# Performance work log

Measured on AMD Instinct MI355X. Metric: run time of the kernel, lower is better.

Reference implementation:

```python
import jax, jax.numpy as jnp
import numpy as np

NQ, NP, E, D, H = 100000, 200000, 500000, 128, 128


def setup_inputs() -> dict:
    key = jax.random.key(0)
    ks = jax.random.split(key, 13)
    ri = lambda k, n: jax.random.randint(k, (E,), 0, n, dtype=jnp.int32)
    return {
        "x_query": jax.random.normal(ks[0], (NQ, D), jnp.float32),
        "x_product": jax.random.normal(ks[1], (NP, D), jnp.float32),
        # [layer, relation, in, out]; relations ordered as ALL_TYPES:
        # 0=Click(Q->P), 1=reverse_Click(P->Q), 2=reverse_QueryResult(P->Q), 3=QueryResult(Q->P)
        "W_self": jax.random.normal(ks[2], (2, 4, D, H), jnp.float32) / np.sqrt(D).astype(np.float32),
        "W_neigh": jax.random.normal(ks[3], (2, 4, D, H), jnp.float32) / np.sqrt(D).astype(np.float32),
        "bias": jax.random.normal(ks[4], (2, 4, H), jnp.float32) * 0.01,
        "click_src": ri(ks[5], NQ), "click_dst": ri(ks[6], NP),
        "qres_src": ri(ks[7], NQ), "qres_dst": ri(ks[8], NP),
        "rclick_src": ri(ks[9], NP), "rclick_dst": ri(ks[10], NQ),
        "rqres_src": ri(ks[11], NP), "rqres_dst": ri(ks[12], NQ),
    }


def _sage(h_src, h_dst, src, dst, n_dst, Ws, Wn, b):
    # DGL SAGEConv 'mean': fc_self(h_dst) + fc_neigh(mean over in-neighbors) + bias
    msum = jax.ops.segment_sum(h_src[src], dst, num_segments=n_dst)  # [n_dst, D]
    deg = jax.ops.segment_sum(jnp.ones(src.shape, h_src.dtype), dst, num_segments=n_dst)
    mean = msum / jnp.maximum(deg, 1.0)[:, None]  # zero-degree nodes get 0
    return h_dst @ Ws + mean @ Wn + b


def reference(x_query, x_product, W_self, W_neigh, bias,
              click_src, click_dst, qres_src, qres_dst,
              rclick_src, rclick_dst, rqres_src, rqres_dst):
    hQ, hP = x_query, x_product
    for l in range(2):
        # HeteroGraphConv aggregate='sum' over relations sharing a dst type
        newP = (_sage(hQ, hP, click_src, click_dst, NP, W_self[l, 0], W_neigh[l, 0], bias[l, 0])
                + _sage(hQ, hP, qres_src, qres_dst, NP, W_self[l, 3], W_neigh[l, 3], bias[l, 3]))
        newQ = (_sage(hP, hQ, rclick_src, rclick_dst, NQ, W_self[l, 1], W_neigh[l, 1], bias[l, 1])
                + _sage(hP, hQ, rqres_src, rqres_dst, NQ, W_self[l, 2], W_neigh[l, 2], bias[l, 2]))
        if l == 0:  # ReLU on all ntypes except after last layer
            newQ, newP = jax.nn.relu(newQ), jax.nn.relu(newP)
        hQ, hP = newQ, newP
    return hQ, hP
```

## Files before the change

kernel.cpp:

```cpp
#include <hip/hip_runtime.h>
#include <hip/hip_bf16.h>

typedef __hip_bfloat16 bf16;
typedef __attribute__((ext_vector_type(8))) short bfrag8;
typedef __attribute__((ext_vector_type(4))) float facc4;

#define NQ_ 100000
#define NP_ 200000
#define NE_ 500000

static __device__ __forceinline__ short f2bf_bits(float f) {
    bf16 h = __float2bfloat16(f);
    short r;
    __builtin_memcpy(&r, &h, 2);
    return r;
}

static __device__ __forceinline__ float bfbits2f(unsigned u) {
    return __builtin_bit_cast(float, u);
}

static __device__ __forceinline__ void store_val(bf16* p, float v) { *p = __float2bfloat16(v); }
static __device__ __forceinline__ void store_val(float* p, float v) { *p = v; }

__global__ void cast_all(const float* __restrict__ xq, const float* __restrict__ xp,
                         bf16* __restrict__ xqb, bf16* __restrict__ xpb) {
    int i = blockIdx.x * blockDim.x + threadIdx.x;
    const int nq4 = NQ_ * 32;
    float4 v;
    short4 o;
    if (i < nq4) {
        v = reinterpret_cast<const float4*>(xq)[i];
        o.x = f2bf_bits(v.x); o.y = f2bf_bits(v.y); o.z = f2bf_bits(v.z); o.w = f2bf_bits(v.w);
        reinterpret_cast<short4*>(xqb)[i] = o;
    } else {
        int j = i - nq4;
        if (j >= NP_ * 32) return;
        v = reinterpret_cast<const float4*>(xp)[j];
        o.x = f2bf_bits(v.x); o.y = f2bf_bits(v.y); o.z = f2bf_bits(v.z); o.w = f2bf_bits(v.w);
        reinterpret_cast<short4*>(xpb)[j] = o;
    }
}

__global__ void prep_weights(const float* __restrict__ Wself, const float* __restrict__ Wneigh,
                             bf16* __restrict__ Wt) {
    int g = blockIdx.x * blockDim.x + threadIdx.x;
    if (g >= 12 * 16384) return;
    int m = g >> 14;
    int rem = g & 16383;
    int n = rem >> 7, k = rem & 127;
    int l = m / 6, t = (m / 3) % 2, s = m % 3;
    int rA = (t == 0) ? 0 : 1;
    int rB = (t == 0) ? 3 : 2;
    float v;
    if (s == 0) {
        v = Wself[((size_t)(l * 4 + rA) * 128 + k) * 128 + n]
          + Wself[((size_t)(l * 4 + rB) * 128 + k) * 128 + n];
    } else {
        int r = (s == 1) ? rA : rB;
        v = Wneigh[((size_t)(l * 4 + r) * 128 + k) * 128 + n];
    }
    Wt[(size_t)m * 16384 + n * 128 + k] = __float2bfloat16(v);
}

__global__ void prep_bias(const float* __restrict__ bias, float* __restrict__ bsum) {
    int g = blockIdx.x * blockDim.x + threadIdx.x;
    if (g >= 512) return;
    int l = g >> 8, t = (g >> 7) & 1, n = g & 127;
    int rA = (t == 0) ? 0 : 1;
    int rB = (t == 0) ? 3 : 2;
    bsum[g] = bias[(l * 4 + rA) * 128 + n] + bias[(l * 4 + rB) * 128 + n];
}


#define NE4_ (NE_ / 4)

__global__ void deg_count_all(const int* __restrict__ cdst, const int* __restrict__ qdst,
                              const int* __restrict__ rcdst, const int* __restrict__ rqdst,
                              int* __restrict__ degAll) {
    int t = blockIdx.x * blockDim.x + threadIdx.x;
    if (t >= 4 * NE4_) return;
    int rel = t / NE4_;
    int er = (t - rel * NE4_) * 4;
    const int* dsts; int base;
    if (rel == 0)      { dsts = cdst;  base = 0; }
    else if (rel == 1) { dsts = qdst;  base = NP_; }
    else if (rel == 2) { dsts = rcdst; base = 2 * NP_; }
    else               { dsts = rqdst; base = 2 * NP_ + NQ_; }
    int4 d4 = *reinterpret_cast<const int4*>(dsts + er);
    atomicAdd(degAll + base + d4.x, 1);
    atomicAdd(degAll + base + d4.y, 1);
    atomicAdd(degAll + base + d4.z, 1);
    atomicAdd(degAll + base + d4.w, 1);
}

__global__ void scan1(const int* __restrict__ deg, int* __restrict__ offs,
                      int* __restrict__ partials, int n) {
    __shared__ int sdata[256];
    int base = blockIdx.x * 1024;
    int t = threadIdx.x;
    int v[4]; int s = 0;
    for (int j = 0; j < 4; ++j) {
        int i = base + t * 4 + j;
        v[j] = (i < n) ? deg[i] : 0;
        s += v[j];
    }
    sdata[t] = s;
    __syncthreads();
    for (int d2 = 1; d2 < 256; d2 <<= 1) {
        int x = (t >= d2) ? sdata[t - d2] : 0;
        __syncthreads();
        sdata[t] += x;
        __syncthreads();
    }
    int excl = sdata[t] - s;
    if (t == 255) partials[blockIdx.x] = sdata[255];
    int run = excl;
    for (int j = 0; j < 4; ++j) {
        int i = base + t * 4 + j;
        if (i < n) offs[i] = run;
        run += v[j];
    }
}

__global__ void scan2(int* __restrict__ partials, int nparts) {
    __shared__ int sdata[256];
    int t = threadIdx.x;
    int v[4]; int s = 0;
    for (int j = 0; j < 4; ++j) {
        int i = t * 4 + j;
        v[j] = (i < nparts) ? partials[i] : 0;
        s += v[j];
    }
    sdata[t] = s;
    __syncthreads();
    for (int d2 = 1; d2 < 256; d2 <<= 1) {
        int x = (t >= d2) ? sdata[t - d2] : 0;
        __syncthreads();
        sdata[t] += x;
        __syncthreads();
    }
    int excl = sdata[t] - s;
    int run = excl;
    for (int j = 0; j < 4; ++j) {
        int i = t * 4 + j;
        if (i < nparts) partials[i] = run;
        run += v[j];
    }
}

__global__ void scan3(int* __restrict__ offs, int* __restrict__ cur,
                      const int* __restrict__ partials, int n) {
    int i = blockIdx.x * blockDim.x + threadIdx.x;
    if (i < n) {
        int v = offs[i] + partials[i >> 10];
        offs[i] = v;
        cur[i] = v;
    }
}

__global__ void csr_fill_all(const int* __restrict__ csrc, const int* __restrict__ cdst,
                             const int* __restrict__ qsrc, const int* __restrict__ qdst,
                             const int* __restrict__ rcsrc, const int* __restrict__ rcdst,
                             const int* __restrict__ rqsrc, const int* __restrict__ rqdst,
                             int* __restrict__ curAll, int* __restrict__ bukAll) {
    int t = blockIdx.x * blockDim.x + threadIdx.x;
    if (t >= 4 * NE4_) return;
    int rel = t / NE4_;
    int er = (t - rel * NE4_) * 4;
    const int* srcs; const int* dsts; int base;
    if (rel == 0)      { srcs = csrc;  dsts = cdst;  base = 0; }
    else if (rel == 1) { srcs = qsrc;  dsts = qdst;  base = NP_; }
    else if (rel == 2) { srcs = rcsrc; dsts = rcdst; base = 2 * NP_; }
    else               { srcs = rqsrc; dsts = rqdst; base = 2 * NP_ + NQ_; }
    int4 d4 = *reinterpret_cast<const int4*>(dsts + er);
    int4 s4 = *reinterpret_cast<const int4*>(srcs + er);
    int p0 = atomicAdd(curAll + base + d4.x, 1);
    int p1 = atomicAdd(curAll + base + d4.y, 1);
    int p2 = atomicAdd(curAll + base + d4.z, 1);
    int p3 = atomicAdd(curAll + base + d4.w, 1);
    bukAll[p0] = s4.x;
    bukAll[p1] = s4.y;
    bukAll[p2] = s4.z;
    bukAll[p3] = s4.w;
}

__global__ __launch_bounds__(256, 8)
void gather_all(const bf16* __restrict__ hQ, const bf16* __restrict__ hP,
                const int* __restrict__ bukAll, const int* __restrict__ offAll,
                const int* __restrict__ degAll, bf16* __restrict__ meanAll) {
    const int tid = threadIdx.x;
    const int lane = tid & 63;
    const int g = lane >> 4;
    const int li = lane & 15;
    const int w = blockIdx.x * 16 + (tid >> 6) * 4 + g;
    const bf16* h = (w < 2 * NP_) ? hQ : hP;
    const int beg = offAll[w];
    const int cnt = degAll[w];

    float a0 = 0.f, a1 = 0.f, a2 = 0.f, a3 = 0.f, a4 = 0.f, a5 = 0.f, a6 = 0.f, a7 = 0.f;

    int myidx = (li < cnt) ? bukAll[beg + li] : 0;
    const int c16 = (cnt < 16) ? cnt : 16;
    const int last = c16 - 1;
    for (int i = 0; i < c16; i += 4) {
#pragma unroll
        for (int j = 0; j < 4; ++j) {
            int idx = i + j;
            int src_lane = g * 16 + ((idx < c16) ? idx : last);
            float m = (idx < c16) ? 1.0f : 0.0f;
            int s_ = __shfl(myidx, src_lane);
            int4 v = reinterpret_cast<const int4*>(h + (size_t)s_ * 128)[li];
            unsigned u0 = (unsigned)v.x, u1 = (unsigned)v.y, u2 = (unsigned)v.z, u3 = (unsigned)v.w;
            a0 = fmaf(bfbits2f(u0 << 16), m, a0);
            a1 = fmaf(bfbits2f(u0 & 0xffff0000u), m, a1);
            a2 = fmaf(bfbits2f(u1 << 16), m, a2);
            a3 = fmaf(bfbits2f(u1 & 0xffff0000u), m, a3);
            a4 = fmaf(bfbits2f(u2 << 16), m, a4);
            a5 = fmaf(bfbits2f(u2 & 0xffff0000u), m, a5);
            a6 = fmaf(bfbits2f(u3 << 16), m, a6);
            a7 = fmaf(bfbits2f(u3 & 0xffff0000u), m, a7);
        }
    }
    for (int i = 16; i < cnt; ++i) {
        int s_ = bukAll[beg + i];
        int4 v = reinterpret_cast<const int4*>(h + (size_t)s_ * 128)[li];
        unsigned u0 = (unsigned)v.x, u1 = (unsigned)v.y, u2 = (unsigned)v.z, u3 = (unsigned)v.w;
        a0 += bfbits2f(u0 << 16);
        a1 += bfbits2f(u0 & 0xffff0000u);
        a2 += bfbits2f(u1 << 16);
        a3 += bfbits2f(u1 & 0xffff0000u);
        a4 += bfbits2f(u2 << 16);
        a5 += bfbits2f(u2 & 0xffff0000u);
        a6 += bfbits2f(u3 << 16);
        a7 += bfbits2f(u3 & 0xffff0000u);
    }

    float r = (cnt > 0) ? (1.0f / (float)cnt) : 0.0f;
    unsigned o0 = ((unsigned)(unsigned short)f2bf_bits(a1 * r) << 16) | (unsigned short)f2bf_bits(a0 * r);
    unsigned o1 = ((unsigned)(unsigned short)f2bf_bits(a3 * r) << 16) | (unsigned short)f2bf_bits(a2 * r);
    unsigned o2 = ((unsigned)(unsigned short)f2bf_bits(a5 * r) << 16) | (unsigned short)f2bf_bits(a4 * r);
    unsigned o3 = ((unsigned)(unsigned short)f2bf_bits(a7 * r) << 16) | (unsigned short)f2bf_bits(a6 * r);
    int4 ov;
    ov.x = (int)o0; ov.y = (int)o1; ov.z = (int)o2; ov.w = (int)o3;
    reinterpret_cast<int4*>(meanAll + (size_t)w * 128)[li] = ov;
}

template <typename OT>
__global__ __launch_bounds__(256, 3)
void sage_all(const bf16* __restrict__ hQin, const bf16* __restrict__ hPin,
              const bf16* __restrict__ meanAll, const bf16* __restrict__ WtL,
              const float* __restrict__ bsumL,
              OT* __restrict__ outQ, OT* __restrict__ outP,
              int do_relu, int nblkP) {
    __shared__ short lA[64 * 136];
    const int tid = threadIdx.x;
    const int wave = tid >> 6, lane = tid & 63;
    const int i16 = lane & 15, quad = lane >> 4;

    const bool isP = (int)blockIdx.x < nblkP;
    const int blk = isP ? blockIdx.x : blockIdx.x - nblkP;
    const int row0 = blk * 64;
    const int nrows = isP ? NP_ : NQ_;
    const bf16* hdst = isP ? hPin : hQin;
    const bf16* m1 = meanAll + (isP ? (size_t)0 : (size_t)(2 * NP_)) * 128;
    const bf16* m2 = meanAll + (isP ? (size_t)NP_ : (size_t)(2 * NP_ + NQ_)) * 128;
    const bf16* Wt3 = WtL + (size_t)(isP ? 0 : 3) * 16384;
    const float* bs = bsumL + (isP ? 0 : 128);
    OT* out = isP ? outP : outQ;

    facc4 acc[4][2];
    for (int nt = 0; nt < 2; ++nt) {
        float bv = bs[wave * 32 + nt * 16 + i16];
        for (int mt = 0; mt < 4; ++mt) {
            facc4 a = {bv, bv, bv, bv};
            acc[mt][nt] = a;
        }
    }

    const bf16* Asrc[3] = {hdst, m1, m2};
#pragma unroll
    for (int s = 0; s < 3; ++s) {
        __syncthreads();
        {
            const bf16* A = Asrc[s];
            for (int j = 0; j < 4; ++j) {
                int c = j * 256 + tid;
                int r = c >> 4, k = (c & 15) * 8;
                int grow = row0 + r;
                int4 v = {0, 0, 0, 0};
                if (grow < nrows)
                    v = reinterpret_cast<const int4*>(A)[((size_t)grow * 128 + k) >> 3];
                *reinterpret_cast<int4*>(&lA[r * 136 + k]) = v;
            }
        }
        __syncthreads();
        const bf16* Ws = Wt3 + (size_t)s * 16384;
#pragma unroll
        for (int k0 = 0; k0 < 128; k0 += 32) {
            bfrag8 a[4], b[2];
            for (int mt = 0; mt < 4; ++mt)
                a[mt] = *reinterpret_cast<const bfrag8*>(&lA[(mt * 16 + i16) * 136 + k0 + quad * 8]);
            for (int nt = 0; nt < 2; ++nt)
                b[nt] = *reinterpret_cast<const bfrag8*>(
                    Ws + (size_t)(wave * 32 + nt * 16 + i16) * 128 + k0 + quad * 8);
            for (int mt = 0; mt < 4; ++mt)
                for (int nt = 0; nt < 2; ++nt)
                    acc[mt][nt] = __builtin_amdgcn_mfma_f32_16x16x32_bf16(a[mt], b[nt], acc[mt][nt], 0, 0, 0);
        }
    }

    for (int mt = 0; mt < 4; ++mt) {
        for (int nt = 0; nt < 2; ++nt) {
            int n = wave * 32 + nt * 16 + i16;
            for (int r = 0; r < 4; ++r) {
                int m = mt * 16 + quad * 4 + r;
                int grow = row0 + m;
                if (grow < nrows) {
                    float v = acc[mt][nt][r];
                    if (do_relu) v = fmaxf(v, 0.0f);
                    store_val(out + (size_t)grow * 128 + n, v);
                }
            }
        }
    }
}


extern "C" void kernel_launch(void* const* d_in, const int* in_sizes, int n_in,
                              void* d_out, int out_size, void* d_ws, size_t ws_size,
                              hipStream_t stream) {
    const float* xq     = (const float*)d_in[0];
    const float* xp     = (const float*)d_in[1];
    const float* Wself  = (const float*)d_in[2];
    const float* Wneigh = (const float*)d_in[3];
    const float* bias   = (const float*)d_in[4];
    const int* csrc  = (const int*)d_in[5];
    const int* cdst  = (const int*)d_in[6];
    const int* qsrc  = (const int*)d_in[7];
    const int* qdst  = (const int*)d_in[8];
    const int* rcsrc = (const int*)d_in[9];
    const int* rcdst = (const int*)d_in[10];
    const int* rqsrc = (const int*)d_in[11];
    const int* rqdst = (const int*)d_in[12];

    const int NDST = 2 * NP_ + 2 * NQ_;

    char* w = (char*)d_ws;
    bf16* xqb    = (bf16*)w;  w += (size_t)NQ_ * 128 * 2;
    bf16* xpb    = (bf16*)w;  w += (size_t)NP_ * 128 * 2;
    bf16* hQ1    = (bf16*)w;  w += (size_t)NQ_ * 128 * 2;
    bf16* hP1    = (bf16*)w;  w += (size_t)NP_ * 128 * 2;
    bf16* meanAll = (bf16*)w; w += (size_t)NDST * 128 * 2;
    bf16* Wt     = (bf16*)w;  w += (size_t)12 * 16384 * 2;
    float* bsum  = (float*)w; w += 512 * 4;
    int* degAll  = (int*)w;   w += (size_t)NDST * 4;
    int* offAll  = (int*)w;   w += (size_t)NDST * 4;
    int* curAll  = (int*)w;   w += (size_t)NDST * 4;
    int* bukAll  = (int*)w;   w += (size_t)4 * NE_ * 4;
    int* partials = (int*)w;  w += 1024 * 4;

    float* outQ = (float*)d_out;
    float* outP = outQ + (size_t)NQ_ * 128;

    cast_all<<<((NQ_ + NP_) * 32 + 255) / 256, 256, 0, stream>>>(xq, xp, xqb, xpb);
    prep_weights<<<768, 256, 0, stream>>>(Wself, Wneigh, Wt);
    prep_bias<<<2, 256, 0, stream>>>(bias, bsum);

    hipMemsetAsync(degAll, 0, (size_t)NDST * 4, stream);
    deg_count_all<<<(4 * NE4_ + 255) / 256, 256, 0, stream>>>(cdst, qdst, rcdst, rqdst, degAll);
    int nparts = (NDST + 1023) / 1024;
    scan1<<<nparts, 256, 0, stream>>>(degAll, offAll, partials, NDST);
    scan2<<<1, 256, 0, stream>>>(partials, nparts);
    scan3<<<(NDST + 255) / 256, 256, 0, stream>>>(offAll, curAll, partials, NDST);
    csr_fill_all<<<(4 * NE4_ + 255) / 256, 256, 0, stream>>>(csrc, cdst, qsrc, qdst,
                                                             rcsrc, rcdst, rqsrc, rqdst,
                                                             curAll, bukAll);

    const int nblkP = (NP_ + 63) / 64;
    const int nblkQ = (NQ_ + 63) / 64;
    const int gather_blocks = NDST / 16;

    for (int l = 0; l < 2; ++l) {
        const bf16* hQin = l ? hQ1 : xqb;
        const bf16* hPin = l ? hP1 : xpb;
        const bf16* WtL = Wt + (size_t)l * 6 * 16384;
        const float* bL = bsum + l * 256;

        gather_all<<<gather_blocks, 256, 0, stream>>>(hQin, hPin, bukAll, offAll, degAll, meanAll);

        if (l == 0)
            sage_all<bf16><<<nblkP + nblkQ, 256, 0, stream>>>(hQin, hPin, meanAll, WtL, bL,
                                                              hQ1, hP1, 1, nblkP);
        else
            sage_all<float><<<nblkP + nblkQ, 256, 0, stream>>>(hQin, hPin, meanAll, WtL, bL,
                                                               outQ, outP, 0, nblkP);
    }
}
```

Before: 897.6 us.

## Fuse preprocessing launches and record per-edge ranks to drop second atomic pass

Merges the cast and degree-count kernels into one launch, and the CSR fill, weight prep and bias prep into another, cutting the launch count. The degree-count pass now saves each edge's atomic return value as its rank, so the fill pass writes to offset+rank with no second round of atomics and scan3 no longer copies a cursor array. The cost is an extra 8 MB rank buffer that must be written and read back, and edges are now handled one per thread instead of four per thread with int4 loads.

```diff
diff --git a/kernel.cpp b/kernel.cpp
--- a/kernel.cpp
+++ b/kernel.cpp
@@ -8,6 +8,11 @@
 #define NQ_ 100000
 #define NP_ 200000
 #define NE_ 500000
+
+#define CAST_BLOCKS 37500
+#define EDGE_BLOCKS 7813
+#define PREPW_BLOCKS 768
+#define PREPB_BLOCKS 2
 
 static __device__ __forceinline__ short f2bf_bits(float f) {
     bf16 h = __float2bfloat16(f);
@@ -23,76 +28,40 @@
 static __device__ __forceinline__ void store_val(bf16* p, float v) { *p = __float2bfloat16(v); }
 static __device__ __forceinline__ void store_val(float* p, float v) { *p = v; }
 
-__global__ void cast_all(const float* __restrict__ xq, const float* __restrict__ xp,
-                         bf16* __restrict__ xqb, bf16* __restrict__ xpb) {
-    int i = blockIdx.x * blockDim.x + threadIdx.x;
-    const int nq4 = NQ_ * 32;
-    float4 v;
-    short4 o;
-    if (i < nq4) {
-        v = reinterpret_cast<const float4*>(xq)[i];
-        o.x = f2bf_bits(v.x); o.y = f2bf_bits(v.y); o.z = f2bf_bits(v.z); o.w = f2bf_bits(v.w);
-        reinterpret_cast<short4*>(xqb)[i] = o;
-    } else {
-        int j = i - nq4;
-        if (j >= NP_ * 32) return;
-        v = reinterpret_cast<const float4*>(xp)[j];
-        o.x = f2bf_bits(v.x); o.y = f2bf_bits(v.y); o.z = f2bf_bits(v.z); o.w = f2bf_bits(v.w);
-        reinterpret_cast<short4*>(xpb)[j] = o;
-    }
-}
-
-__global__ void prep_weights(const float* __restrict__ Wself, const float* __restrict__ Wneigh,
-                             bf16* __restrict__ Wt) {
-    int g = blockIdx.x * blockDim.x + threadIdx.x;
-    if (g >= 12 * 16384) return;
-    int m = g >> 14;
-    int rem = g & 16383;
-    int n = rem >> 7, k = rem & 127;
-    int l = m / 6, t = (m / 3) % 2, s = m % 3;
-    int rA = (t == 0) ? 0 : 1;
-    int rB = (t == 0) ? 3 : 2;
-    float v;
-    if (s == 0) {
-        v = Wself[((size_t)(l * 4 + rA) * 128 + k) * 128 + n]
-          + Wself[((size_t)(l * 4 + rB) * 128 + k) * 128 + n];
-    } else {
-        int r = (s == 1) ? rA : rB;
-        v = Wneigh[((size_t)(l * 4 + r) * 128 + k) * 128 + n];
-    }
-    Wt[(size_t)m * 16384 + n * 128 + k] = __float2bfloat16(v);
-}
-
-__global__ void prep_bias(const float* __restrict__ bias, float* __restrict__ bsum) {
-    int g = blockIdx.x * blockDim.x + threadIdx.x;
-    if (g >= 512) return;
-    int l = g >> 8, t = (g >> 7) & 1, n = g & 127;
-    int rA = (t == 0) ? 0 : 1;
-    int rB = (t == 0) ? 3 : 2;
-    bsum[g] = bias[(l * 4 + rA) * 128 + n] + bias[(l * 4 + rB) * 128 + n];
-}
-
-
-#define NE4_ (NE_ / 4)
-
-__global__ void deg_count_all(const int* __restrict__ cdst, const int* __restrict__ qdst,
-                              const int* __restrict__ rcdst, const int* __restrict__ rqdst,
-                              int* __restrict__ degAll) {
-    int t = blockIdx.x * blockDim.x + threadIdx.x;
-    if (t >= 4 * NE4_) return;
-    int rel = t / NE4_;
-    int er = (t - rel * NE4_) * 4;
-    const int* dsts; int base;
-    if (rel == 0)      { dsts = cdst;  base = 0; }
-    else if (rel == 1) { dsts = qdst;  base = NP_; }
-    else if (rel == 2) { dsts = rcdst; base = 2 * NP_; }
-    else               { dsts = rqdst; base = 2 * NP_ + NQ_; }
-    int4 d4 = *reinterpret_cast<const int4*>(dsts + er);
-    atomicAdd(degAll + base + d4.x, 1);
-    atomicAdd(degAll + base + d4.y, 1);
-    atomicAdd(degAll + base + d4.z, 1);
-    atomicAdd(degAll + base + d4.w, 1);
-}
+__global__ void fused_cast_deg(const float* __restrict__ xq, const float* __restrict__ xp,
+                               bf16* __restrict__ xqb, bf16* __restrict__ xpb,
+                               const int* __restrict__ cdst, const int* __restrict__ qdst,
+                               const int* __restrict__ rcdst, const int* __restrict__ rqdst,
+                               int* __restrict__ degAll, int* __restrict__ rankAll) {
+    if ((int)blockIdx.x < CAST_BLOCKS) {
+        int i = blockIdx.x * blockDim.x + threadIdx.x;
+        const int nq4 = NQ_ * 32;
+        float4 v;
+        short4 o;
+        if (i < nq4) {
+            v = reinterpret_cast<const float4*>(xq)[i];
+            o.x = f2bf_bits(v.x); o.y = f2bf_bits(v.y); o.z = f2bf_bits(v.z); o.w = f2bf_bits(v.w);
+            reinterpret_cast<short4*>(xqb)[i] = o;
+        } else {
+            int j = i - nq4;
+            v = reinterpret_cast<const float4*>(xp)[j];
+            o.x = f2bf_bits(v.x); o.y = f2bf_bits(v.y); o.z = f2bf_bits(v.z); o.w = f2bf_bits(v.w);
+            reinterpret_cast<short4*>(xpb)[j] = o;
+        }
+        return;
+    }
+    int e = (blockIdx.x - CAST_BLOCKS) * blockDim.x + threadIdx.x;
+    if (e >= 4 * NE_) return;
+    int rel = e / NE_;
+    int er = e - rel * NE_;
+    int d, base;
+    if (rel == 0)      { d = cdst[er];  base = 0; }
+    else if (rel == 1) { d = qdst[er];  base = NP_; }
+    else if (rel == 2) { d = rcdst[er]; base = 2 * NP_; }
+    else               { d = rqdst[er]; base = 2 * NP_ + NQ_; }
+    rankAll[e] = atomicAdd(degAll + base + d, 1);
+}
+
 
 __global__ void scan1(const int* __restrict__ deg, int* __restrict__ offs,
                       int* __restrict__ partials, int n) {
@@ -149,40 +118,60 @@
     }
 }
 
-__global__ void scan3(int* __restrict__ offs, int* __restrict__ cur,
-                      const int* __restrict__ partials, int n) {
+__global__ void scan3(int* __restrict__ offs, const int* __restrict__ partials, int n) {
     int i = blockIdx.x * blockDim.x + threadIdx.x;
-    if (i < n) {
-        int v = offs[i] + partials[i >> 10];
-        offs[i] = v;
-        cur[i] = v;
-    }
-}
-
-__global__ void csr_fill_all(const int* __restrict__ csrc, const int* __restrict__ cdst,
-                             const int* __restrict__ qsrc, const int* __restrict__ qdst,
-                             const int* __restrict__ rcsrc, const int* __restrict__ rcdst,
-                             const int* __restrict__ rqsrc, const int* __restrict__ rqdst,
-                             int* __restrict__ curAll, int* __restrict__ bukAll) {
-    int t = blockIdx.x * blockDim.x + threadIdx.x;
-    if (t >= 4 * NE4_) return;
-    int rel = t / NE4_;
-    int er = (t - rel * NE4_) * 4;
-    const int* srcs; const int* dsts; int base;
-    if (rel == 0)      { srcs = csrc;  dsts = cdst;  base = 0; }
-    else if (rel == 1) { srcs = qsrc;  dsts = qdst;  base = NP_; }
-    else if (rel == 2) { srcs = rcsrc; dsts = rcdst; base = 2 * NP_; }
-    else               { srcs = rqsrc; dsts = rqdst; base = 2 * NP_ + NQ_; }
-    int4 d4 = *reinterpret_cast<const int4*>(dsts + er);
-    int4 s4 = *reinterpret_cast<const int4*>(srcs + er);
-    int p0 = atomicAdd(curAll + base + d4.x, 1);
-    int p1 = atomicAdd(curAll + base + d4.y, 1);
-    int p2 = atomicAdd(curAll + base + d4.z, 1);
-    int p3 = atomicAdd(curAll + base + d4.w, 1);
-    bukAll[p0] = s4.x;
-    bukAll[p1] = s4.y;
-    bukAll[p2] = s4.z;
-    bukAll[p3] = s4.w;
+    if (i < n) offs[i] += partials[i >> 10];
+}
+
+__global__ void fused_fill_prep(const int* __restrict__ csrc, const int* __restrict__ cdst,
+                                const int* __restrict__ qsrc, const int* __restrict__ qdst,
+                                const int* __restrict__ rcsrc, const int* __restrict__ rcdst,
+                                const int* __restrict__ rqsrc, const int* __restrict__ rqdst,
+                                const int* __restrict__ offAll, const int* __restrict__ rankAll,
+                                int* __restrict__ bukAll,
+                                const float* __restrict__ Wself, const float* __restrict__ Wneigh,
+                                bf16* __restrict__ Wt,
+                                const float* __restrict__ bias, float* __restrict__ bsum) {
+    if ((int)blockIdx.x < EDGE_BLOCKS) {
+        int e = blockIdx.x * blockDim.x + threadIdx.x;
+        if (e >= 4 * NE_) return;
+        int rel = e / NE_;
+        int er = e - rel * NE_;
+        int d, s, base;
+        if (rel == 0)      { d = cdst[er];  s = csrc[er];  base = 0; }
+        else if (rel == 1) { d = qdst[er];  s = qsrc[er];  base = NP_; }
+        else if (rel == 2) { d = rcdst[er]; s = rcsrc[er]; base = 2 * NP_; }
+        else               { d = rqdst[er]; s = rqsrc[er]; base = 2 * NP_ + NQ_; }
+        bukAll[offAll[base + d] + rankAll[e]] = s;
+        return;
+    }
+    if ((int)blockIdx.x < EDGE_BLOCKS + PREPW_BLOCKS) {
+        int g = (blockIdx.x - EDGE_BLOCKS) * blockDim.x + threadIdx.x;
+        int m = g >> 14;
+        int rem = g & 16383;
+        int n = rem >> 7, k = rem & 127;
+        int l = m / 6, t = (m / 3) % 2, s = m % 3;
+        int rA = (t == 0) ? 0 : 1;
+        int rB = (t == 0) ? 3 : 2;
+        float v;
+        if (s == 0) {
+            v = Wself[((size_t)(l * 4 + rA) * 128 + k) * 128 + n]
+              + Wself[((size_t)(l * 4 + rB) * 128 + k) * 128 + n];
+        } else {
+            int r = (s == 1) ? rA : rB;
+            v = Wneigh[((size_t)(l * 4 + r) * 128 + k) * 128 + n];
+        }
+        Wt[(size_t)m * 16384 + n * 128 + k] = __float2bfloat16(v);
+        return;
+    }
+    {
+        int g = (blockIdx.x - EDGE_BLOCKS - PREPW_BLOCKS) * blockDim.x + threadIdx.x;
+        if (g >= 512) return;
+        int l = g >> 8, t = (g >> 7) & 1, n = g & 127;
+        int rA = (t == 0) ? 0 : 1;
+        int rB = (t == 0) ? 3 : 2;
+        bsum[g] = bias[(l * 4 + rA) * 128 + n] + bias[(l * 4 + rB) * 128 + n];
+    }
 }
 
 __global__ __launch_bounds__(256, 8)
@@ -356,26 +345,23 @@
     float* bsum  = (float*)w; w += 512 * 4;
     int* degAll  = (int*)w;   w += (size_t)NDST * 4;
     int* offAll  = (int*)w;   w += (size_t)NDST * 4;
-    int* curAll  = (int*)w;   w += (size_t)NDST * 4;
+    int* rankAll = (int*)w;   w += (size_t)4 * NE_ * 4;
     int* bukAll  = (int*)w;   w += (size_t)4 * NE_ * 4;
     int* partials = (int*)w;  w += 1024 * 4;
 
     float* outQ = (float*)d_out;
     float* outP = outQ + (size_t)NQ_ * 128;
 
-    cast_all<<<((NQ_ + NP_) * 32 + 255) / 256, 256, 0, stream>>>(xq, xp, xqb, xpb);
-    prep_weights<<<768, 256, 0, stream>>>(Wself, Wneigh, Wt);
-    prep_bias<<<2, 256, 0, stream>>>(bias, bsum);
-
     hipMemsetAsync(degAll, 0, (size_t)NDST * 4, stream);
-    deg_count_all<<<(4 * NE4_ + 255) / 256, 256, 0, stream>>>(cdst, qdst, rcdst, rqdst, degAll);
+    fused_cast_deg<<<CAST_BLOCKS + EDGE_BLOCKS, 256, 0, stream>>>(
+        xq, xp, xqb, xpb, cdst, qdst, rcdst, rqdst, degAll, rankAll);
     int nparts = (NDST + 1023) / 1024;
     scan1<<<nparts, 256, 0, stream>>>(degAll, offAll, partials, NDST);
     scan2<<<1, 256, 0, stream>>>(partials, nparts);
-    scan3<<<(NDST + 255) / 256, 256, 0, stream>>>(offAll, curAll, partials, NDST);
-    csr_fill_all<<<(4 * NE4_ + 255) / 256, 256, 0, stream>>>(csrc, cdst, qsrc, qdst,
-                                                             rcsrc, rcdst, rqsrc, rqdst,
-                                                             curAll, bukAll);
+    scan3<<<(NDST + 255) / 256, 256, 0, stream>>>(offAll, partials, NDST);
+    fused_fill_prep<<<EDGE_BLOCKS + PREPW_BLOCKS + PREPB_BLOCKS, 256, 0, stream>>>(
+        csrc, cdst, qsrc, qdst, rcsrc, rcdst, rqsrc, rqdst,
+        offAll, rankAll, bukAll, Wself, Wneigh, Wt, bias, bsum);
 
     const int nblkP = (NP_ + 63) / 64;
     const int nblkQ = (NQ_ + 63) / 64;
```

Measured after the change: 781.3 us. 13.0% less time.
